# Kernel optimization log

Hardware: AMD Instinct MI355X
Metric: run time of the kernel (lower is better)

The kernel has to match this reference:

```python
import jax, jax.numpy as jnp
import numpy as np
import math

HID = 1024
SLOTS = 64
KD = 32
B = 16384


def _normalize(v):
    # matches torch F.normalize(dim=-1, eps=1e-12)
    return v / jnp.clip(jnp.linalg.norm(v, axis=-1, keepdims=True), 1e-12)


def setup_inputs() -> dict:
    key = jax.random.key(0)
    ks = jax.random.split(key, 10)
    sc = lambda k, shape, s: jax.random.normal(k, shape, dtype=jnp.float32) * s
    return {
        "x": jax.random.normal(ks[0], (B, HID), dtype=jnp.float32),
        "key_w": sc(ks[1], (KD, HID), 0.02),
        "out_w": sc(ks[2], (HID, 2 * HID), 0.02),
        "out_b": jnp.zeros((HID,), jnp.float32),
        "gate_w": sc(ks[3], (HID, 2 * HID), 0.02),
        "gate_b": jnp.zeros((HID,), jnp.float32),
        "ln_g": jnp.ones((HID,), jnp.float32),
        "ln_b": jnp.zeros((HID,), jnp.float32),
        "pos_table": sc(ks[4], (SLOTS, KD), 1.0),
        "mem_keys": sc(ks[5], (SLOTS, KD), 0.02),
        "mem_vals": sc(ks[6], (SLOTS, HID), 0.5),
        "mem_age": jax.random.uniform(ks[7], (SLOTS,), dtype=jnp.float32) * 300.0,
        "mem_conf": jax.random.uniform(ks[8], (SLOTS,), dtype=jnp.float32),
        "slot_order": jnp.arange(SLOTS, dtype=jnp.int32),
    }


def reference(x, key_w, out_w, out_b, gate_w, gate_b, ln_g, ln_b,
              pos_table, mem_keys, mem_vals, mem_age, mem_conf, slot_order):
    # key projection  [B, KD]
    qk = x @ key_w.T
    # positional embedding of slot order, added to memory keys
    pos_emb = pos_table[slot_order % SLOTS]            # [S, KD]
    keys_with_pos = _normalize(mem_keys + 0.1 * pos_emb)
    query_norm = _normalize(qk)
    sim = (query_norm @ keys_with_pos.T) / math.sqrt(KD)  # [B, S]

    # multi-term salience (SalienceScorer.score with type_weight=0.8)
    recency = jnp.exp(-mem_age / 200.0)                # [S]
    freq = jnp.clip(mem_age, 1.0)                      # age.clamp(min=1) used as frequency
    freq_norm = jnp.log(freq + 1.0) / (jnp.log(freq.max() + 2.0) + 1e-8)
    bias = 0.2 * recency + 0.15 * freq_norm + 0.1 * mem_conf + 0.1 * 0.8  # [S]
    sal = jnp.clip(0.45 * sim + bias[None, :], 0.0, 1.0)

    attn = jax.nn.softmax(sal, axis=-1)                # [B, S]
    retrieved = attn @ mem_vals                        # [B, HID]

    combined = jnp.concatenate([x, retrieved], axis=-1)  # [B, 2*HID]
    gate_val = jax.nn.sigmoid(combined @ gate_w.T + gate_b)
    blended = gate_val * retrieved + (1.0 - gate_val) * x
    h = jax.nn.gelu(combined @ out_w.T + out_b, approximate=False)  # eval: dropout is identity
    y = h + blended

    # LayerNorm (eps=1e-5)
    mu = y.mean(axis=-1, keepdims=True)
    var = ((y - mu) ** 2).mean(axis=-1, keepdims=True)
    return (y - mu) / jnp.sqrt(var + 1e-5) * ln_g + ln_b
```

## Files before the change

kernel.cpp:

```cpp
#include <hip/hip_runtime.h>
#include <hip/hip_bf16.h>
#include <math.h>


typedef float    f32x4 __attribute__((ext_vector_type(4)));
typedef short    s16x8 __attribute__((ext_vector_type(8)));
typedef unsigned short u16;
typedef unsigned short u16x8 __attribute__((ext_vector_type(8)));

#define MFMA_BF16(a,b,c) __builtin_amdgcn_mfma_f32_16x16x32_bf16((a),(b),(c),0,0,0)

__device__ __forceinline__ void async16(void* lds, const void* g) {
  __builtin_amdgcn_global_load_lds((const __attribute__((address_space(1))) void*)g,
                                   (__attribute__((address_space(3))) void*)lds, 16, 0, 0);
}

__device__ __forceinline__ u16 f2bf(float f) {
  unsigned u = __float_as_uint(f);
  u += 0x7fffu + ((u >> 16) & 1u);
  return (u16)(u >> 16);
}
__device__ __forceinline__ float bf2f(u16 h) {
  return __uint_as_float(((unsigned)h) << 16);
}
__device__ __forceinline__ int ocol_of(int p) { return ((p >> 5) << 4) + (p & 15); }

__global__ __launch_bounds__(256) void k_front(
    const float* __restrict__ x, const float* __restrict__ gate_w,
    const float* __restrict__ out_w, const float* __restrict__ key_w,
    const float* __restrict__ mem_vals, const float* __restrict__ mem_keys,
    const float* __restrict__ pos_table, const int* __restrict__ slot_order,
    const float* __restrict__ mem_age, const float* __restrict__ mem_conf,
    u16* __restrict__ A, u16* __restrict__ Wcat, u16* __restrict__ Vcat) {
  const int b = blockIdx.x, tid = threadIdx.x;

  if (b >= 288) {
    const int pb = (b - 288) * 64;
    for (int e = tid; e < 64*64; e += 256) {
      int pl = e >> 6, s = e & 63;
      int p = pb + pl;
      Vcat[(size_t)p*64 + s] = f2bf(mem_vals[(size_t)s*1024 + ocol_of(p)]);
    }
    __shared__ __align__(16) u16 sW[64*80];
    __shared__ __align__(16) u16 sV[64*80];
    const int lane = tid & 63, w = tid >> 6;
    const int ln15 = lane & 15, hi = lane >> 4;
    f32x4 acc[4];
    #pragma unroll
    for (int n = 0; n < 4; n++) acc[n] = {0.f,0.f,0.f,0.f};
    for (int kt = 0; kt < 16; ++kt) {
      #pragma unroll
      for (int j = 0; j < 4; j++) {
        int idx = tid + j*256;
        int row = idx >> 4, g4 = idx & 15;
        int p = pb + row;
        const float* wsrc = ((p >> 4) & 1) ? out_w : gate_w;
        float4 v = *(const float4*)&wsrc[(size_t)ocol_of(p)*2048 + 1024 + kt*64 + g4*4];
        ushort4 o; o.x=f2bf(v.x); o.y=f2bf(v.y); o.z=f2bf(v.z); o.w=f2bf(v.w);
        *(ushort4*)&sW[row*80 + g4*4] = o;
        float4 u = *(const float4*)&mem_vals[(size_t)row*1024 + kt*64 + g4*4];
        ushort4 p2; p2.x=f2bf(u.x); p2.y=f2bf(u.y); p2.z=f2bf(u.z); p2.w=f2bf(u.w);
        *(ushort4*)&sV[row*80 + g4*4] = p2;
      }
      __syncthreads();
      #pragma unroll
      for (int kk = 0; kk < 2; kk++) {
        int kb = kk*32 + hi*8;
        s16x8 a = *(const s16x8*)&sW[(w*16 + ln15)*80 + kb];
        #pragma unroll
        for (int n = 0; n < 4; n++) {
          s16x8 bv = *(const s16x8*)&sV[(n*16 + ln15)*80 + kb];
          acc[n] = MFMA_BF16(a, bv, acc[n]);
        }
      }
      __syncthreads();
    }
    #pragma unroll
    for (int n = 0; n < 4; n++)
      #pragma unroll
      for (int i = 0; i < 4; i++) {
        int p = pb + w*16 + hi*4 + i;
        Wcat[(size_t)p*1088 + 1024 + n*16 + ln15] = f2bf(acc[n][i]);
      }
    return;
  }

  if (b >= 256) {
    for (int g = (b-256)*256 + tid; g < 524288; g += 32*256) {
      float4 v; int t, pb2;
      if (g < 262144) { t = g;          v = *(const float4*)&gate_w[(size_t)(t>>8)*2048 + (t&255)*4]; pb2 = 0; }
      else            { t = g - 262144; v = *(const float4*)&out_w [(size_t)(t>>8)*2048 + (t&255)*4]; pb2 = 16; }
      int row = t >> 8, grp = t & 255;
      int p = ((row>>4)<<5) + pb2 + (row&15);
      ushort4 o; o.x=f2bf(v.x); o.y=f2bf(v.y); o.z=f2bf(v.z); o.w=f2bf(v.w);
      *(ushort4*)(Wcat + ((size_t)p*1088 + grp*4)) = o;
    }
    return;
  }

  __shared__ __align__(16) u16 sX[64*72];
  __shared__ __align__(16) u16 sWk[32*72];
  __shared__ float sQK[64*33];
  __shared__ float sK[64*33];
  __shared__ float sBias[64];
  __shared__ float sQn[64*32];

  const int lane = tid & 63, w = tid >> 6;
  const int ln15 = lane & 15, hi = lane >> 4;
  const size_t r0 = (size_t)b * 64;

  if (tid < 64) {
    int s = tid;
    float age  = mem_age[s];
    float freq = fmaxf(age, 1.0f);
    float fm = freq;
    #pragma unroll
    for (int o = 32; o; o >>= 1) fm = fmaxf(fm, __shfl_xor(fm, o));
    float freq_norm = logf(freq + 1.0f) / (logf(fm + 2.0f) + 1e-8f);
    float recency = expf(-age * (1.0f/200.0f));
    sBias[s] = 0.2f*recency + 0.15f*freq_norm + 0.1f*mem_conf[s] + 0.08f;

    int idx = slot_order[s] & 63;
    float k[32]; float ss = 0.f;
    #pragma unroll
    for (int d = 0; d < 32; d++) {
      float v = mem_keys[s*32+d] + 0.1f*pos_table[idx*32+d];
      k[d] = v; ss += v*v;
    }
    float inv = 1.0f / fmaxf(sqrtf(ss), 1e-12f);
    #pragma unroll
    for (int d = 0; d < 32; d++) sK[s*33+d] = k[d]*inv;
  }

  f32x4 acc0 = {0.f,0.f,0.f,0.f}, acc1 = {0.f,0.f,0.f,0.f};
  const int xrow = tid >> 4, xc4 = tid & 15;
  for (int k0 = 0; k0 < 1024; k0 += 64) {
    #pragma unroll
    for (int j = 0; j < 4; j++) {
      int row = xrow + j*16;
      float4 v = *(const float4*)&x[(r0+row)*1024 + k0 + xc4*4];
      ushort4 o; o.x=f2bf(v.x); o.y=f2bf(v.y); o.z=f2bf(v.z); o.w=f2bf(v.w);
      *(ushort4*)&sX[row*72 + xc4*4] = o;
      *(ushort4*)&A[(r0+row)*1088 + k0 + xc4*4] = o;
    }
    #pragma unroll
    for (int j = 0; j < 2; j++) {
      int idx = tid + j*256;
      int row = idx >> 4, c4 = idx & 15;
      float4 v = *(const float4*)&key_w[(size_t)row*1024 + k0 + c4*4];
      ushort4 o; o.x=f2bf(v.x); o.y=f2bf(v.y); o.z=f2bf(v.z); o.w=f2bf(v.w);
      *(ushort4*)&sWk[row*72 + c4*4] = o;
    }
    __syncthreads();
    #pragma unroll
    for (int kk = 0; kk < 2; kk++) {
      int kb = kk*32 + hi*8;
      s16x8 a  = *(const s16x8*)&sX[(w*16 + ln15)*72 + kb];
      s16x8 b0 = *(const s16x8*)&sWk[ln15*72 + kb];
      s16x8 b1 = *(const s16x8*)&sWk[(16+ln15)*72 + kb];
      acc0 = MFMA_BF16(a, b0, acc0);
      acc1 = MFMA_BF16(a, b1, acc1);
    }
    __syncthreads();
  }
  #pragma unroll
  for (int i = 0; i < 4; i++) {
    sQK[(w*16 + hi*4 + i)*33 + ln15]      = acc0[i];
    sQK[(w*16 + hi*4 + i)*33 + 16 + ln15] = acc1[i];
  }
  __syncthreads();

  int d = lane & 31;
  for (int j = 0; j < 16; j++) {
    int rl = w*16 + j;
    float v = sQK[rl*33 + d];
    float sq = v*v;
    #pragma unroll
    for (int o = 16; o; o >>= 1) sq += __shfl_xor(sq, o);
    float qn = v / fmaxf(sqrtf(sq), 1e-12f);
    if (lane < 32) sQn[rl*32 + d] = qn;
    float accs = 0.f;
    #pragma unroll
    for (int dd = 0; dd < 32; dd++) accs += sK[lane*33+dd] * sQn[rl*32+dd];
    float sim = accs * 0.17677669529663687f;
    float sal = fminf(fmaxf(0.45f*sim + sBias[lane], 0.0f), 1.0f);
    float mx = sal;
    #pragma unroll
    for (int o = 32; o; o >>= 1) mx = fmaxf(mx, __shfl_xor(mx, o));
    float e = expf(sal - mx);
    float sm = e;
    #pragma unroll
    for (int o = 32; o; o >>= 1) sm += __shfl_xor(sm, o);
    A[(r0 + rl)*1088 + 1024 + lane] = f2bf(e / sm);
  }
}

__global__ __launch_bounds__(1024, 2) void k_gemm(
    const u16* __restrict__ A, const u16* __restrict__ Wcat,
    const u16* __restrict__ Vcat, const float* __restrict__ out_b,
    const float* __restrict__ gate_b, u16* __restrict__ yb) {
  __shared__ __align__(16) u16 sA[16384];
  __shared__ __align__(16) u16 sB[16384];

  const int tid = threadIdx.x, lane = tid & 63, w = tid >> 6;
  const int ln15 = lane & 15, hi = lane >> 4, p7 = ln15 & 7;
  const int wm = w >> 2, wn = w & 3;

  const int colblk = blockIdx.x & 7;
  const int rowblk = blockIdx.x >> 3;
  const size_t r0 = (size_t)rowblk * 256;
  const size_t c0 = (size_t)colblk * 256;

  const u16* gA = A    + r0 * 1088;
  const u16* gB = Wcat + c0 * 1088;
  const u16* gV = Vcat + c0 * 64;

  int offA[2], offB[2], offV[2];
  #pragma unroll
  for (int j = 0; j < 2; j++) {
    int c = tid + j*1024, row = c >> 3, pc = c & 7;
    int sw = ((pc ^ (row & 7)) << 3);
    offA[j] = row*1088 + sw;
    offB[j] = row*1088 + sw;
    offV[j] = row*64   + sw;
  }

  const int ck0 = (hi ^ p7) * 8;
  const int ck1 = ((4 | hi) ^ p7) * 8;
  const int arow = (wm*64 + ln15) * 64;
  const int brow = (wn*64 + ln15) * 64;

  f32x4 acc[4][4], accr[4][2];
  #pragma unroll
  for (int m = 0; m < 4; m++) {
    #pragma unroll
    for (int n = 0; n < 4; n++) acc[m][n] = {0.f, 0.f, 0.f, 0.f};
    accr[m][0] = {0.f,0.f,0.f,0.f}; accr[m][1] = {0.f,0.f,0.f,0.f};
  }

  #pragma unroll 1
  for (int kt = 0; kt < 17; ++kt) {
    const int ko = kt * 64;
    #pragma unroll
    for (int j = 0; j < 2; j++) {
      async16(&sA[(tid + j*1024)*8], gA + offA[j] + ko);
      async16(&sB[(tid + j*1024)*8], gB + offB[j] + ko);
    }
    __syncthreads();
    #pragma unroll
    for (int kk = 0; kk < 2; kk++) {
      const int ck = kk ? ck1 : ck0;
      s16x8 af[4], bfr[4];
      #pragma unroll
      for (int m = 0; m < 4; m++) af[m]  = *(const s16x8*)&sA[arow + m*1024 + ck];
      #pragma unroll
      for (int n = 0; n < 4; n++) bfr[n] = *(const s16x8*)&sB[brow + n*1024 + ck];
      #pragma unroll
      for (int m = 0; m < 4; m++)
        #pragma unroll
        for (int n = 0; n < 4; n++)
          acc[m][n] = MFMA_BF16(af[m], bfr[n], acc[m][n]);
    }
    __syncthreads();
  }

  #pragma unroll
  for (int j = 0; j < 2; j++) async16(&sB[(tid + j*1024)*8], gV + offV[j]);
  __syncthreads();
  #pragma unroll
  for (int kk = 0; kk < 2; kk++) {
    const int ck = kk ? ck1 : ck0;
    s16x8 af[4], bf0, bf1;
    #pragma unroll
    for (int m = 0; m < 4; m++) af[m] = *(const s16x8*)&sA[arow + m*1024 + ck];
    bf0 = *(const s16x8*)&sB[brow + ck];
    bf1 = *(const s16x8*)&sB[brow + 2*1024 + ck];
    #pragma unroll
    for (int m = 0; m < 4; m++) {
      accr[m][0] = MFMA_BF16(af[m], bf0, accr[m][0]);
      accr[m][1] = MFMA_BF16(af[m], bf1, accr[m][1]);
    }
  }

  #pragma unroll
  for (int s = 0; s < 2; s++) {
    int ocol = colblk*128 + wn*32 + s*16 + ln15;
    float gbv = gate_b[ocol], obv = out_b[ocol];
    #pragma unroll
    for (int m = 0; m < 4; m++) {
      #pragma unroll
      for (int i = 0; i < 4; i++) {
        size_t r = r0 + wm*64 + m*16 + hi*4 + i;
        float gg = acc[m][s*2+0][i] + gbv;
        float go = acc[m][s*2+1][i] + obv;
        float h  = 0.5f*go*(1.0f + erff(go*0.70710678118654752f));
        float sg = 1.0f/(1.0f + __expf(-gg));
        float rv = accr[m][s][i];
        float xv = bf2f(A[r*1088 + ocol]);
        yb[r*1024 + ocol] = f2bf(h + sg*rv + (1.0f - sg)*xv);
      }
    }
  }
}

__global__ __launch_bounds__(256) void k_ln(const u16* __restrict__ yb,
                                            const float* __restrict__ g,
                                            const float* __restrict__ b,
                                            float* __restrict__ out) {
  int row  = blockIdx.x*4 + (threadIdx.x >> 6);
  int lane = threadIdx.x & 63;
  const u16* p = yb + (size_t)row*1024 + lane*16;
  u16x8 h0 = *(const u16x8*)p;
  u16x8 h1 = *(const u16x8*)(p + 8);
  float v[16];
  #pragma unroll
  for (int i = 0; i < 8; i++) { v[i] = bf2f((u16)h0[i]); v[8+i] = bf2f((u16)h1[i]); }
  float s = 0.f;
  #pragma unroll
  for (int i = 0; i < 16; i++) s += v[i];
  #pragma unroll
  for (int o = 32; o; o >>= 1) s += __shfl_xor(s, o);
  float mu = s * (1.0f/1024.0f);
  float vs = 0.f;
  #pragma unroll
  for (int i = 0; i < 16; i++) { float d0 = v[i]-mu; vs += d0*d0; }
  #pragma unroll
  for (int o = 32; o; o >>= 1) vs += __shfl_xor(vs, o);
  float inv = 1.0f / sqrtf(vs*(1.0f/1024.0f) + 1e-5f);
  const float4* gp = (const float4*)(g + lane*16);
  const float4* bp = (const float4*)(b + lane*16);
  float4* op = (float4*)(out + (size_t)row*1024 + lane*16);
  #pragma unroll
  for (int i = 0; i < 4; i++) {
    float4 gv = gp[i], bv = bp[i], o4;
    o4.x = (v[i*4+0]-mu)*inv*gv.x + bv.x;
    o4.y = (v[i*4+1]-mu)*inv*gv.y + bv.y;
    o4.z = (v[i*4+2]-mu)*inv*gv.z + bv.z;
    o4.w = (v[i*4+3]-mu)*inv*gv.w + bv.w;
    op[i] = o4;
  }
}

extern "C" void kernel_launch(void* const* d_in, const int* in_sizes, int n_in,
                              void* d_out, int out_size, void* d_ws, size_t ws_size,
                              hipStream_t stream) {
  const float* x         = (const float*)d_in[0];
  const float* key_w     = (const float*)d_in[1];
  const float* out_w     = (const float*)d_in[2];
  const float* out_b     = (const float*)d_in[3];
  const float* gate_w    = (const float*)d_in[4];
  const float* gate_b    = (const float*)d_in[5];
  const float* ln_g      = (const float*)d_in[6];
  const float* ln_b      = (const float*)d_in[7];
  const float* pos_table = (const float*)d_in[8];
  const float* mem_keys  = (const float*)d_in[9];
  const float* mem_vals  = (const float*)d_in[10];
  const float* mem_age   = (const float*)d_in[11];
  const float* mem_conf  = (const float*)d_in[12];
  const int*   slot_order= (const int*)d_in[13];

  char* ws = (char*)d_ws;
  u16*   A    = (u16*)(ws + 0);
  u16*   Wcat = (u16*)(ws + 36700160);
  u16*   Vcat = (u16*)(ws + 41943040);
  u16*   yb   = (u16*)(ws + 42205184);
  float* y    = (float*)d_out;

  hipLaunchKernelGGL(k_front, dim3(320),  dim3(256),  0, stream,
                     x, gate_w, out_w, key_w, mem_vals, mem_keys, pos_table,
                     slot_order, mem_age, mem_conf, A, Wcat, Vcat);
  hipLaunchKernelGGL(k_gemm,  dim3(512),  dim3(1024), 0, stream,
                     A, Wcat, Vcat, out_b, gate_b, yb);
  hipLaunchKernelGGL(k_ln,    dim3(4096), dim3(256),  0, stream,
                     yb, ln_g, ln_b, y);
}
```

Baseline: 174.7 us.

## Reuse staged x tile from LDS and stage epilogue output for coalesced stores

Result: slower. 220.9 us (+26.4%).

```diff
diff --git a/kernel.cpp b/kernel.cpp
--- a/kernel.cpp
+++ b/kernel.cpp
@@ -199,8 +199,9 @@
     const u16* __restrict__ A, const u16* __restrict__ Wcat,
     const u16* __restrict__ Vcat, const float* __restrict__ out_b,
     const float* __restrict__ gate_b, u16* __restrict__ yb) {
-  __shared__ __align__(16) u16 sA[16384];
-  __shared__ __align__(16) u16 sB[16384];
+  __shared__ __align__(16) u16 smem[32768];
+  u16* sA = smem;
+  u16* sB = smem + 16384;
 
   const int tid = threadIdx.x, lane = tid & 63, w = tid >> 6;
   const int ln15 = lane & 15, hi = lane >> 4, p7 = ln15 & 7;
@@ -237,6 +238,7 @@
     for (int n = 0; n < 4; n++) acc[m][n] = {0.f, 0.f, 0.f, 0.f};
     accr[m][0] = {0.f,0.f,0.f,0.f}; accr[m][1] = {0.f,0.f,0.f,0.f};
   }
+  float xv[2][4][4];
 
   #pragma unroll 1
   for (int kt = 0; kt < 17; ++kt) {
@@ -261,6 +263,19 @@
         for (int n = 0; n < 4; n++)
           acc[m][n] = MFMA_BF16(af[m], bfr[n], acc[m][n]);
     }
+    if ((kt >> 1) == colblk && (wn >> 1) == (kt & 1)) {
+      #pragma unroll
+      for (int s = 0; s < 2; s++) {
+        int c = (wn & 1)*32 + s*16 + ln15;
+        #pragma unroll
+        for (int m = 0; m < 4; m++)
+          #pragma unroll
+          for (int i = 0; i < 4; i++) {
+            int r = wm*64 + m*16 + hi*4 + i;
+            xv[s][m][i] = bf2f(sA[r*64 + (((c >> 3) ^ (r & 7)) << 3) + (c & 7)]);
+          }
+      }
+    }
     __syncthreads();
   }
 
@@ -281,25 +296,36 @@
       accr[m][1] = MFMA_BF16(af[m], bf1, accr[m][1]);
     }
   }
+  __syncthreads();
 
   #pragma unroll
   for (int s = 0; s < 2; s++) {
-    int ocol = colblk*128 + wn*32 + s*16 + ln15;
+    int c = wn*32 + s*16 + ln15;
+    int ocol = colblk*128 + c;
     float gbv = gate_b[ocol], obv = out_b[ocol];
     #pragma unroll
     for (int m = 0; m < 4; m++) {
       #pragma unroll
       for (int i = 0; i < 4; i++) {
-        size_t r = r0 + wm*64 + m*16 + hi*4 + i;
+        int r = wm*64 + m*16 + hi*4 + i;
         float gg = acc[m][s*2+0][i] + gbv;
         float go = acc[m][s*2+1][i] + obv;
         float h  = 0.5f*go*(1.0f + erff(go*0.70710678118654752f));
         float sg = 1.0f/(1.0f + __expf(-gg));
-        float rv = accr[m][s][i];
-        float xv = bf2f(A[r*1088 + ocol]);
-        yb[r*1024 + ocol] = f2bf(h + sg*rv + (1.0f - sg)*xv);
+        float yv = h + sg*accr[m][s][i] + (1.0f - sg)*xv[s][m][i];
+        smem[r*128 + (c ^ ((r & 15) << 3))] = f2bf(yv);
       }
     }
+  }
+  __syncthreads();
+
+  #pragma unroll
+  for (int j = 0; j < 4; j++) {
+    int chunk = tid + j*1024;
+    int row = chunk >> 4;
+    int cc = (chunk & 15) << 3;
+    u16x8 v = *(const u16x8*)&smem[row*128 + (cc ^ ((row & 15) << 3))];
+    *(u16x8*)&yb[(r0 + row)*1024 + colblk*128 + cc] = v;
   }
 }
 
```
